# Kernel optimization log

Measured on AMD Instinct MI355X. Metric: run time of the kernel, lower is better.

The kernel has to match this reference:

```python
import jax, jax.numpy as jnp
import numpy as np

N = 400000   # active voxels (submanifold: N' == N)
K3 = 27      # kernel_size**3
D = 64       # in_channels
DP = 64      # out_channels


def setup_inputs() -> dict:
    key = jax.random.key(0)
    k1, k2, k3 = jax.random.split(key, 3)
    feats = jax.random.normal(k1, (N, D), dtype=jnp.float32)
    # neighbor index table: indices[k, n] = row of feats contributing at kernel
    # offset k for output site n; negative would mean 'no neighbor' (masked).
    indices = jax.random.randint(k2, (K3, N), 0, N, dtype=jnp.int64)
    weight = jax.random.normal(k3, (K3, D, DP), dtype=jnp.float32)
    return {"feats": feats, "indices": indices, "weight": weight}


def reference(feats, indices, weight):
    # Submanifold sparse conv as implicit GEMM:
    #   out[n] = sum_k feats[indices[k, n]] @ weight[k]   (skip indices < 0)
    # Scan over the K^3 kernel offsets (fixed, small) to avoid materializing
    # the full [K3, N, D] gathered tensor.
    n_out = indices.shape[1]
    dp = weight.shape[2]

    def body(acc, kw):
        idx, w = kw                                   # idx: [N'], w: [D, DP]
        valid = (idx >= 0)[:, None]                   # [N', 1]
        g = jnp.where(valid, feats[jnp.maximum(idx, 0)], 0.0)  # [N', D]
        return acc + g @ w, None

    init = jnp.zeros((n_out, dp), dtype=feats.dtype)
    out, _ = jax.lax.scan(body, init, (indices, weight))
    return out
```

## Files before the change

kernel.cpp:

```cpp
#include <hip/hip_runtime.h>
#include <hip/hip_bf16.h>
#include <stdint.h>

typedef __bf16 bf16_t;
typedef bf16_t bf16x8 __attribute__((ext_vector_type(8)));
typedef float f32x4 __attribute__((ext_vector_type(4)));

#define D_IN 64
#define D_OUT 64
#define BM 128
#define NTHREADS 512

#define GLOAD_LDS16(gsrc, ldst)                                                     \
    __builtin_amdgcn_global_load_lds(                                               \
        (const __attribute__((address_space(1))) uint32_t*)(gsrc),                  \
        (__attribute__((address_space(3))) uint32_t*)(ldst), 16, 0, 0)

__device__ __forceinline__ uint32_t swz(int row, int col) {
    return (uint32_t)((row * 128 + col * 2) ^ ((row & 7) << 4));
}

__global__ void convert_feats(const float* __restrict__ feats,
                              bf16_t* __restrict__ fb,
                              int n_elems , int total8 ) {
    int g = blockIdx.x * blockDim.x + threadIdx.x;
    for (; g < total8; g += gridDim.x * blockDim.x) {
        const int e = g * 8;
        bf16x8 v = {};
        if (e < n_elems) {
            f32x4 a = *(const f32x4*)(feats + e);
            f32x4 b = *(const f32x4*)(feats + e + 4);
            #pragma unroll
            for (int i = 0; i < 4; ++i) {
                v[i]     = (bf16_t)a[i];
                v[i + 4] = (bf16_t)b[i];
            }
        }
        *(bf16x8*)(fb + e) = v;
    }
}

__global__ void convert_weight(const float* __restrict__ w,
                               bf16_t* __restrict__ wtb, int k3) {
    const int k = blockIdx.x;
    const int tid = threadIdx.x;
    const int dp = tid >> 3;
    const int cp = tid & 7;
    const int d0 = (cp ^ (dp & 7)) * 8;
    const float* src = w + (size_t)k * (D_IN * D_OUT) + (size_t)d0 * D_OUT + dp;
    bf16x8 v;
    #pragma unroll
    for (int j = 0; j < 8; ++j) v[j] = (bf16_t)src[j * D_OUT];
    *(bf16x8*)((char*)wtb + (size_t)k * 8192 + tid * 16) = v;
}

__global__ __launch_bounds__(NTHREADS, 1) void subm_conv_mfma2(
    const bf16_t* __restrict__ fb,
    const int* __restrict__ indices,
    const bf16_t* __restrict__ wtb,
    float* __restrict__ out,
    int n_vox, int k3)
{
    __shared__ __align__(16) bf16_t As[2][BM * 64];
    __shared__ __align__(16) bf16_t Bs[2][64 * 64];

    const int tid  = threadIdx.x;
    const int lane = tid & 63;
    const int wv   = tid >> 6;
    const int l15  = lane & 15;
    const int l4   = lane >> 4;
    const int wr   = (wv >> 1) * 32;
    const int wc   = (wv & 1) * 32;
    const int n0   = blockIdx.x * BM;

    const int rA0 = wv * 16 + (lane >> 3);
    const int rA1 = rA0 + 8;
    const int cp  = lane & 7;
    const uint32_t so0 = (uint32_t)((cp ^ (rA0 & 7)) * 16);
    const uint32_t so1 = (uint32_t)((cp ^ (rA1 & 7)) * 16);

    int ia0 = -1, ia1 = -1;

    #define LOADIDX(kk) do {                                                   \
        const int* ip = indices + (size_t)(kk) * n_vox + n0;                   \
        ia0 = (n0 + rA0 < n_vox) ? ip[rA0] : -1;                               \
        ia1 = (n0 + rA1 < n_vox) ? ip[rA1] : -1;                               \
    } while (0)

    #define STAGE(buf, kk) do {                                                \
                      \
        GLOAD_LDS16((const char*)wtb + (size_t)(kk) * 8192 + tid * 16,         \
                    (char*)&Bs[buf][0] + wv * 1024);                           \
                                   \
        const size_t r0 = (size_t)((ia0 >= 0 && ia0 < n_vox) ? ia0 : n_vox);   \
        const size_t r1 = (size_t)((ia1 >= 0 && ia1 < n_vox) ? ia1 : n_vox);   \
        GLOAD_LDS16((const char*)fb + r0 * 128 + so0,                          \
                    (char*)&As[buf][0] + wv * 2048);                           \
        GLOAD_LDS16((const char*)fb + r1 * 128 + so1,                          \
                    (char*)&As[buf][0] + wv * 2048 + 1024);                    \
    } while (0)

    f32x4 acc[2][2];
    #pragma unroll
    for (int i = 0; i < 2; ++i)
        #pragma unroll
        for (int j = 0; j < 2; ++j)
            acc[i][j] = (f32x4){0.f, 0.f, 0.f, 0.f};

    LOADIDX(0);
    STAGE(0, 0);
    if (k3 > 1) LOADIDX(1);

    for (int k = 0; k < k3; ++k) {
        __syncthreads();

        if (k + 1 < k3) STAGE((k + 1) & 1, k + 1);
        if (k + 2 < k3) LOADIDX(k + 2);

        const char* ab = (const char*)&As[k & 1][0];
        const char* bb = (const char*)&Bs[k & 1][0];
        #pragma unroll
        for (int ks = 0; ks < 2; ++ks) {
            const int kc = ks * 32 + l4 * 8;
            bf16x8 a0 = *(const bf16x8*)(ab + swz(wr + l15,      kc));
            bf16x8 a1 = *(const bf16x8*)(ab + swz(wr + 16 + l15, kc));
            bf16x8 b0 = *(const bf16x8*)(bb + swz(wc + l15,      kc));
            bf16x8 b1 = *(const bf16x8*)(bb + swz(wc + 16 + l15, kc));
            acc[0][0] = __builtin_amdgcn_mfma_f32_16x16x32_bf16(a0, b0, acc[0][0], 0, 0, 0);
            acc[0][1] = __builtin_amdgcn_mfma_f32_16x16x32_bf16(a0, b1, acc[0][1], 0, 0, 0);
            acc[1][0] = __builtin_amdgcn_mfma_f32_16x16x32_bf16(a1, b0, acc[1][0], 0, 0, 0);
            acc[1][1] = __builtin_amdgcn_mfma_f32_16x16x32_bf16(a1, b1, acc[1][1], 0, 0, 0);
        }
    }

    #pragma unroll
    for (int mi = 0; mi < 2; ++mi)
        #pragma unroll
        for (int ni = 0; ni < 2; ++ni)
            #pragma unroll
            for (int j = 0; j < 4; ++j) {
                const int row = n0 + wr + mi * 16 + l4 * 4 + j;
                const int col = wc + ni * 16 + l15;
                if (row < n_vox)
                    out[(size_t)row * D_OUT + col] = acc[mi][ni][j];
            }
    #undef LOADIDX
    #undef STAGE
}

__global__ __launch_bounds__(NTHREADS, 1) void subm_conv_mfma_v1(
    const float* __restrict__ feats,
    const int* __restrict__ indices,
    const float* __restrict__ weight,
    float* __restrict__ out,
    int n_vox, int k3)
{
    __shared__ bf16_t As[BM * 64];
    __shared__ bf16_t Bs[64 * 64];

    const int tid  = threadIdx.x;
    const int lane = tid & 63;
    const int wv   = tid >> 6;
    const int wr   = (wv >> 1) * 32;
    const int wc   = (wv & 1) * 32;
    const int l15  = lane & 15;
    const int l4   = lane >> 4;
    const int n0   = blockIdx.x * BM;

    const int ar = tid >> 2;
    const int ac = (tid & 3) * 16;
    const int bdp = tid & 63;
    const int bd0 = (tid >> 6) * 8;

    f32x4 acc[2][2];
    #pragma unroll
    for (int i = 0; i < 2; ++i)
        #pragma unroll
        for (int j = 0; j < 2; ++j)
            acc[i][j] = (f32x4){0.f, 0.f, 0.f, 0.f};

    for (int k = 0; k < k3; ++k) {
        __syncthreads();
        {
            const int n = n0 + ar;
            int idx = (n < n_vox) ? indices[(size_t)k * n_vox + n] : -1;
            bf16x8 v0 = {}, v1 = {};
            if (idx >= 0) {
                const float* src = feats + (size_t)idx * D_IN + ac;
                f32x4 f0 = *(const f32x4*)(src + 0);
                f32x4 f1 = *(const f32x4*)(src + 4);
                f32x4 f2 = *(const f32x4*)(src + 8);
                f32x4 f3 = *(const f32x4*)(src + 12);
                #pragma unroll
                for (int i = 0; i < 4; ++i) {
                    v0[i]     = (bf16_t)f0[i];
                    v0[i + 4] = (bf16_t)f1[i];
                    v1[i]     = (bf16_t)f2[i];
                    v1[i + 4] = (bf16_t)f3[i];
                }
            }
            *(bf16x8*)((char*)As + swz(ar, ac))     = v0;
            *(bf16x8*)((char*)As + swz(ar, ac + 8)) = v1;
        }
        {
            const float* wsrc = weight + (size_t)k * (D_IN * D_OUT) + (size_t)bd0 * D_OUT + bdp;
            bf16x8 v;
            #pragma unroll
            for (int i = 0; i < 8; ++i) v[i] = (bf16_t)wsrc[i * D_OUT];
            *(bf16x8*)((char*)Bs + swz(bdp, bd0)) = v;
        }
        __syncthreads();
        #pragma unroll
        for (int ks = 0; ks < 2; ++ks) {
            const int kc = ks * 32 + l4 * 8;
            bf16x8 a0 = *(const bf16x8*)((char*)As + swz(wr + l15,      kc));
            bf16x8 a1 = *(const bf16x8*)((char*)As + swz(wr + 16 + l15, kc));
            bf16x8 b0 = *(const bf16x8*)((char*)Bs + swz(wc + l15,      kc));
            bf16x8 b1 = *(const bf16x8*)((char*)Bs + swz(wc + 16 + l15, kc));
            acc[0][0] = __builtin_amdgcn_mfma_f32_16x16x32_bf16(a0, b0, acc[0][0], 0, 0, 0);
            acc[0][1] = __builtin_amdgcn_mfma_f32_16x16x32_bf16(a0, b1, acc[0][1], 0, 0, 0);
            acc[1][0] = __builtin_amdgcn_mfma_f32_16x16x32_bf16(a1, b0, acc[1][0], 0, 0, 0);
            acc[1][1] = __builtin_amdgcn_mfma_f32_16x16x32_bf16(a1, b1, acc[1][1], 0, 0, 0);
        }
    }

    #pragma unroll
    for (int mi = 0; mi < 2; ++mi)
        #pragma unroll
        for (int ni = 0; ni < 2; ++ni)
            #pragma unroll
            for (int j = 0; j < 4; ++j) {
                const int row = n0 + wr + mi * 16 + l4 * 4 + j;
                const int col = wc + ni * 16 + l15;
                if (row < n_vox)
                    out[(size_t)row * D_OUT + col] = acc[mi][ni][j];
            }
}

extern "C" void kernel_launch(void* const* d_in, const int* in_sizes, int n_in,
                              void* d_out, int out_size, void* d_ws, size_t ws_size,
                              hipStream_t stream) {
    const float* feats   = (const float*)d_in[0];
    const int*   indices = (const int*)d_in[1];
    const float* weight  = (const float*)d_in[2];
    float* out = (float*)d_out;

    const int n_vox = in_sizes[0] / D_IN;
    const int k3    = in_sizes[2] / (D_IN * D_OUT);
    const int grid  = (n_vox + BM - 1) / BM;

    const size_t fb_bytes  = (size_t)(n_vox + 1) * D_IN * sizeof(bf16_t);
    const size_t fb_off    = 0;
    const size_t wtb_off   = (fb_bytes + 255) & ~(size_t)255;
    const size_t wtb_bytes = (size_t)k3 * 64 * 64 * sizeof(bf16_t);
    const size_t need      = wtb_off + wtb_bytes;

    if (ws_size >= need) {
        bf16_t* fb  = (bf16_t*)((char*)d_ws + fb_off);
        bf16_t* wtb = (bf16_t*)((char*)d_ws + wtb_off);

        const int n_elems = n_vox * D_IN;
        const int total8  = (n_vox + 1) * (D_IN / 8);
        int cblocks = (total8 + 255) / 256;
        if (cblocks > 2048) cblocks = 2048;
        convert_feats<<<cblocks, 256, 0, stream>>>(feats, fb, n_elems, total8);
        convert_weight<<<k3, 512, 0, stream>>>(weight, wtb, k3);
        subm_conv_mfma2<<<grid, NTHREADS, 0, stream>>>(fb, indices, wtb, out, n_vox, k3);
    } else {
        subm_conv_mfma_v1<<<grid, NTHREADS, 0, stream>>>(feats, indices, weight, out, n_vox, k3);
    }
}
```

Measured before the change: 245.0 us.

## Triple-buffer LDS staging with partial vmcnt waits and MFMA priority

Moves the gather-GEMM kernel from double to triple buffering of the A and B tiles in LDS. Index loads now run four offsets ahead and tile stages two ahead. The full __syncthreads is replaced by an explicit s_waitcnt vmcnt(5) plus a barrier, so later async loads can stay in flight, and s_setprio raises wave priority around the MFMA block. It also raises the launch-bounds occupancy hint to 4 blocks per CU. The aim is to hide more of the random-gather latency, at the cost of extra LDS (72KB per block), which may limit how many blocks fit, and reliance on a hand-counted vmcnt.

```diff
diff --git a/kernel.cpp b/kernel.cpp
--- a/kernel.cpp
+++ b/kernel.cpp
@@ -22,7 +22,7 @@
 
 __global__ void convert_feats(const float* __restrict__ feats,
                               bf16_t* __restrict__ fb,
-                              int n_elems , int total8 ) {
+                              int n_elems, int total8) {
     int g = blockIdx.x * blockDim.x + threadIdx.x;
     for (; g < total8; g += gridDim.x * blockDim.x) {
         const int e = g * 8;
@@ -54,15 +54,15 @@
     *(bf16x8*)((char*)wtb + (size_t)k * 8192 + tid * 16) = v;
 }
 
-__global__ __launch_bounds__(NTHREADS, 1) void subm_conv_mfma2(
+__global__ __launch_bounds__(NTHREADS, 4) void subm_conv_mfma3(
     const bf16_t* __restrict__ fb,
     const int* __restrict__ indices,
     const bf16_t* __restrict__ wtb,
     float* __restrict__ out,
     int n_vox, int k3)
 {
-    __shared__ __align__(16) bf16_t As[2][BM * 64];
-    __shared__ __align__(16) bf16_t Bs[2][64 * 64];
+    __shared__ __align__(16) bf16_t As[3][BM * 64];
+    __shared__ __align__(16) bf16_t Bs[3][64 * 64];
 
     const int tid  = threadIdx.x;
     const int lane = tid & 63;
@@ -79,25 +79,21 @@
     const uint32_t so0 = (uint32_t)((cp ^ (rA0 & 7)) * 16);
     const uint32_t so1 = (uint32_t)((cp ^ (rA1 & 7)) * 16);
 
-    int ia0 = -1, ia1 = -1;
-
-    #define LOADIDX(kk) do {                                                   \
+    #define LOADIDX(kk, j0, j1) do {                                           \
         const int* ip = indices + (size_t)(kk) * n_vox + n0;                   \
-        ia0 = (n0 + rA0 < n_vox) ? ip[rA0] : -1;                               \
-        ia1 = (n0 + rA1 < n_vox) ? ip[rA1] : -1;                               \
+        j0 = (n0 + rA0 < n_vox) ? ip[rA0] : -1;                                \
+        j1 = (n0 + rA1 < n_vox) ? ip[rA1] : -1;                                \
     } while (0)
 
-    #define STAGE(buf, kk) do {                                                \
-                      \
+    #define STAGE(bufi, kk, j0, j1) do {                                       \
         GLOAD_LDS16((const char*)wtb + (size_t)(kk) * 8192 + tid * 16,         \
-                    (char*)&Bs[buf][0] + wv * 1024);                           \
-                                   \
-        const size_t r0 = (size_t)((ia0 >= 0 && ia0 < n_vox) ? ia0 : n_vox);   \
-        const size_t r1 = (size_t)((ia1 >= 0 && ia1 < n_vox) ? ia1 : n_vox);   \
-        GLOAD_LDS16((const char*)fb + r0 * 128 + so0,                          \
-                    (char*)&As[buf][0] + wv * 2048);                           \
-        GLOAD_LDS16((const char*)fb + r1 * 128 + so1,                          \
-                    (char*)&As[buf][0] + wv * 2048 + 1024);                    \
+                    (char*)&Bs[(bufi)][0] + wv * 1024);                        \
+        const size_t r0_ = (size_t)(((j0) >= 0 && (j0) < n_vox) ? (j0) : n_vox); \
+        const size_t r1_ = (size_t)(((j1) >= 0 && (j1) < n_vox) ? (j1) : n_vox); \
+        GLOAD_LDS16((const char*)fb + r0_ * 128 + so0,                         \
+                    (char*)&As[(bufi)][0] + wv * 2048);                        \
+        GLOAD_LDS16((const char*)fb + r1_ * 128 + so1,                         \
+                    (char*)&As[(bufi)][0] + wv * 2048 + 1024);                 \
     } while (0)
 
     f32x4 acc[2][2];
@@ -107,18 +103,40 @@
         for (int j = 0; j < 2; ++j)
             acc[i][j] = (f32x4){0.f, 0.f, 0.f, 0.f};
 
-    LOADIDX(0);
-    STAGE(0, 0);
-    if (k3 > 1) LOADIDX(1);
+    {
+        int p00, p01, p10, p11;
+        LOADIDX(0, p00, p01);
+        const int k1 = (1 < k3) ? 1 : k3 - 1;
+        LOADIDX(k1, p10, p11);
+        STAGE(0, 0, p00, p01);
+        STAGE(1, k1, p10, p11);
+    }
+    int ia_c0, ia_c1, ia_n0, ia_n1;
+    {
+        const int k2 = (2 < k3) ? 2 : k3 - 1;
+        const int k3c = (3 < k3) ? 3 : k3 - 1;
+        LOADIDX(k2, ia_c0, ia_c1);
+        LOADIDX(k3c, ia_n0, ia_n1);
+    }
+
+    int bc = 0;
+    int bs = 2;
 
     for (int k = 0; k < k3; ++k) {
-        __syncthreads();
-
-        if (k + 1 < k3) STAGE((k + 1) & 1, k + 1);
-        if (k + 2 < k3) LOADIDX(k + 2);
-
-        const char* ab = (const char*)&As[k & 1][0];
-        const char* bb = (const char*)&Bs[k & 1][0];
+        asm volatile("s_waitcnt vmcnt(5)" ::: "memory");
+        __builtin_amdgcn_s_barrier();
+
+        int t0, t1;
+        {
+            const int ki = (k + 4 < k3) ? k + 4 : k3 - 1;
+            LOADIDX(ki, t0, t1);
+            const int ks = (k + 2 < k3) ? k + 2 : k3 - 1;
+            STAGE(bs, ks, ia_c0, ia_c1);
+        }
+
+        const char* ab = (const char*)&As[bc][0];
+        const char* bb = (const char*)&Bs[bc][0];
+        __builtin_amdgcn_s_setprio(1);
         #pragma unroll
         for (int ks = 0; ks < 2; ++ks) {
             const int kc = ks * 32 + l4 * 8;
@@ -131,6 +149,11 @@
             acc[1][0] = __builtin_amdgcn_mfma_f32_16x16x32_bf16(a1, b0, acc[1][0], 0, 0, 0);
             acc[1][1] = __builtin_amdgcn_mfma_f32_16x16x32_bf16(a1, b1, acc[1][1], 0, 0, 0);
         }
+        __builtin_amdgcn_s_setprio(0);
+
+        ia_c0 = ia_n0; ia_c1 = ia_n1; ia_n0 = t0; ia_n1 = t1;
+        bc = (bc == 2) ? 0 : bc + 1;
+        bs = (bs == 2) ? 0 : bs + 1;
     }
 
     #pragma unroll
@@ -250,13 +273,12 @@
     const int grid  = (n_vox + BM - 1) / BM;
 
     const size_t fb_bytes  = (size_t)(n_vox + 1) * D_IN * sizeof(bf16_t);
-    const size_t fb_off    = 0;
     const size_t wtb_off   = (fb_bytes + 255) & ~(size_t)255;
     const size_t wtb_bytes = (size_t)k3 * 64 * 64 * sizeof(bf16_t);
     const size_t need      = wtb_off + wtb_bytes;
 
-    if (ws_size >= need) {
-        bf16_t* fb  = (bf16_t*)((char*)d_ws + fb_off);
+    if (ws_size >= need && k3 >= 2) {
+        bf16_t* fb  = (bf16_t*)((char*)d_ws);
         bf16_t* wtb = (bf16_t*)((char*)d_ws + wtb_off);
 
         const int n_elems = n_vox * D_IN;
@@ -265,7 +287,7 @@
         if (cblocks > 2048) cblocks = 2048;
         convert_feats<<<cblocks, 256, 0, stream>>>(feats, fb, n_elems, total8);
         convert_weight<<<k3, 512, 0, stream>>>(weight, wtb, k3);
-        subm_conv_mfma2<<<grid, NTHREADS, 0, stream>>>(fb, indices, wtb, out, n_vox, k3);
+        subm_conv_mfma3<<<grid, NTHREADS, 0, stream>>>(fb, indices, wtb, out, n_vox, k3);
     } else {
         subm_conv_mfma_v1<<<grid, NTHREADS, 0, stream>>>(feats, indices, weight, out, n_vox, k3);
     }
```

Measured after the change: 284.3 us. 1.16x slower.

## Read weight fragments directly from global memory instead of staging through LDS

Applied to the files above, without the earlier changes.

Drops the LDS double buffer for the weight tile. Each wave now loads its B fragments straight from a row-major bf16 weight layout in global memory (likely L2-resident) at the start of each offset iteration. The convert kernel writes that unswizzled layout. This halves LDS traffic and footprint, so launch bounds go to 8 blocks per CU for more occupancy. The cost is redundant global or L2 reads of weights by every block and wave, plus tighter register limits from the higher occupancy bound.

```diff
diff --git a/kernel.cpp b/kernel.cpp
--- a/kernel.cpp
+++ b/kernel.cpp
@@ -22,7 +22,7 @@
 
 __global__ void convert_feats(const float* __restrict__ feats,
                               bf16_t* __restrict__ fb,
-                              int n_elems , int total8 ) {
+                              int n_elems, int total8) {
     int g = blockIdx.x * blockDim.x + threadIdx.x;
     for (; g < total8; g += gridDim.x * blockDim.x) {
         const int e = g * 8;
@@ -41,28 +41,26 @@
 }
 
 __global__ void convert_weight(const float* __restrict__ w,
-                               bf16_t* __restrict__ wtb, int k3) {
+                               bf16_t* __restrict__ wt, int k3) {
     const int k = blockIdx.x;
     const int tid = threadIdx.x;
     const int dp = tid >> 3;
-    const int cp = tid & 7;
-    const int d0 = (cp ^ (dp & 7)) * 8;
+    const int d0 = (tid & 7) * 8;
     const float* src = w + (size_t)k * (D_IN * D_OUT) + (size_t)d0 * D_OUT + dp;
     bf16x8 v;
     #pragma unroll
     for (int j = 0; j < 8; ++j) v[j] = (bf16_t)src[j * D_OUT];
-    *(bf16x8*)((char*)wtb + (size_t)k * 8192 + tid * 16) = v;
-}
-
-__global__ __launch_bounds__(NTHREADS, 1) void subm_conv_mfma2(
+    *(bf16x8*)((char*)wt + (size_t)k * 8192 + dp * 128 + d0 * 2) = v;
+}
+
+__global__ __launch_bounds__(NTHREADS, 8) void subm_conv_hi(
     const bf16_t* __restrict__ fb,
     const int* __restrict__ indices,
-    const bf16_t* __restrict__ wtb,
+    const bf16_t* __restrict__ wt,
     float* __restrict__ out,
     int n_vox, int k3)
 {
     __shared__ __align__(16) bf16_t As[2][BM * 64];
-    __shared__ __align__(16) bf16_t Bs[2][64 * 64];
 
     const int tid  = threadIdx.x;
     const int lane = tid & 63;
@@ -88,15 +86,11 @@
     } while (0)
 
     #define STAGE(buf, kk) do {                                                \
-                      \
-        GLOAD_LDS16((const char*)wtb + (size_t)(kk) * 8192 + tid * 16,         \
-                    (char*)&Bs[buf][0] + wv * 1024);                           \
-                                   \
-        const size_t r0 = (size_t)((ia0 >= 0 && ia0 < n_vox) ? ia0 : n_vox);   \
-        const size_t r1 = (size_t)((ia1 >= 0 && ia1 < n_vox) ? ia1 : n_vox);   \
-        GLOAD_LDS16((const char*)fb + r0 * 128 + so0,                          \
+        const size_t r0_ = (size_t)((ia0 >= 0 && ia0 < n_vox) ? ia0 : n_vox);  \
+        const size_t r1_ = (size_t)((ia1 >= 0 && ia1 < n_vox) ? ia1 : n_vox);  \
+        GLOAD_LDS16((const char*)fb + r0_ * 128 + so0,                         \
                     (char*)&As[buf][0] + wv * 2048);                           \
-        GLOAD_LDS16((const char*)fb + r1 * 128 + so1,                          \
+        GLOAD_LDS16((const char*)fb + r1_ * 128 + so1,                         \
                     (char*)&As[buf][0] + wv * 2048 + 1024);                    \
     } while (0)
 
@@ -114,22 +108,35 @@
     for (int k = 0; k < k3; ++k) {
         __syncthreads();
 
+        const char* wb = (const char*)wt + (size_t)k * 8192
+                       + (size_t)(wc + l15) * 128 + l4 * 16;
+        bf16x8 b00 = *(const bf16x8*)(wb);
+        bf16x8 b01 = *(const bf16x8*)(wb + 64);
+        bf16x8 b10 = *(const bf16x8*)(wb + 2048);
+        bf16x8 b11 = *(const bf16x8*)(wb + 2048 + 64);
+        __builtin_amdgcn_sched_barrier(0);
+
         if (k + 1 < k3) STAGE((k + 1) & 1, k + 1);
         if (k + 2 < k3) LOADIDX(k + 2);
 
         const char* ab = (const char*)&As[k & 1][0];
-        const char* bb = (const char*)&Bs[k & 1][0];
-        #pragma unroll
-        for (int ks = 0; ks < 2; ++ks) {
-            const int kc = ks * 32 + l4 * 8;
+        {
+            const int kc = l4 * 8;
             bf16x8 a0 = *(const bf16x8*)(ab + swz(wr + l15,      kc));
             bf16x8 a1 = *(const bf16x8*)(ab + swz(wr + 16 + l15, kc));
-            bf16x8 b0 = *(const bf16x8*)(bb + swz(wc + l15,      kc));
-            bf16x8 b1 = *(const bf16x8*)(bb + swz(wc + 16 + l15, kc));
-            acc[0][0] = __builtin_amdgcn_mfma_f32_16x16x32_bf16(a0, b0, acc[0][0], 0, 0, 0);
-            acc[0][1] = __builtin_amdgcn_mfma_f32_16x16x32_bf16(a0, b1, acc[0][1], 0, 0, 0);
-            acc[1][0] = __builtin_amdgcn_mfma_f32_16x16x32_bf16(a1, b0, acc[1][0], 0, 0, 0);
-            acc[1][1] = __builtin_amdgcn_mfma_f32_16x16x32_bf16(a1, b1, acc[1][1], 0, 0, 0);
+            acc[0][0] = __builtin_amdgcn_mfma_f32_16x16x32_bf16(a0, b00, acc[0][0], 0, 0, 0);
+            acc[0][1] = __builtin_amdgcn_mfma_f32_16x16x32_bf16(a0, b10, acc[0][1], 0, 0, 0);
+            acc[1][0] = __builtin_amdgcn_mfma_f32_16x16x32_bf16(a1, b00, acc[1][0], 0, 0, 0);
+            acc[1][1] = __builtin_amdgcn_mfma_f32_16x16x32_bf16(a1, b10, acc[1][1], 0, 0, 0);
+        }
+        {
+            const int kc = 32 + l4 * 8;
+            bf16x8 a0 = *(const bf16x8*)(ab + swz(wr + l15,      kc));
+            bf16x8 a1 = *(const bf16x8*)(ab + swz(wr + 16 + l15, kc));
+            acc[0][0] = __builtin_amdgcn_mfma_f32_16x16x32_bf16(a0, b01, acc[0][0], 0, 0, 0);
+            acc[0][1] = __builtin_amdgcn_mfma_f32_16x16x32_bf16(a0, b11, acc[0][1], 0, 0, 0);
+            acc[1][0] = __builtin_amdgcn_mfma_f32_16x16x32_bf16(a1, b01, acc[1][0], 0, 0, 0);
+            acc[1][1] = __builtin_amdgcn_mfma_f32_16x16x32_bf16(a1, b11, acc[1][1], 0, 0, 0);
         }
     }
 
@@ -148,14 +155,14 @@
     #undef STAGE
 }
 
-__global__ __launch_bounds__(NTHREADS, 1) void subm_conv_mfma_v1(
+__global__ __launch_bounds__(512, 1) void subm_conv_mfma_v1(
     const float* __restrict__ feats,
     const int* __restrict__ indices,
     const float* __restrict__ weight,
     float* __restrict__ out,
     int n_vox, int k3)
 {
-    __shared__ bf16_t As[BM * 64];
+    __shared__ bf16_t As[128 * 64];
     __shared__ bf16_t Bs[64 * 64];
 
     const int tid  = threadIdx.x;
@@ -165,7 +172,7 @@
     const int wc   = (wv & 1) * 32;
     const int l15  = lane & 15;
     const int l4   = lane >> 4;
-    const int n0   = blockIdx.x * BM;
+    const int n0   = blockIdx.x * 128;
 
     const int ar = tid >> 2;
     const int ac = (tid & 3) * 16;
@@ -250,23 +257,22 @@
     const int grid  = (n_vox + BM - 1) / BM;
 
     const size_t fb_bytes  = (size_t)(n_vox + 1) * D_IN * sizeof(bf16_t);
-    const size_t fb_off    = 0;
-    const size_t wtb_off   = (fb_bytes + 255) & ~(size_t)255;
-    const size_t wtb_bytes = (size_t)k3 * 64 * 64 * sizeof(bf16_t);
-    const size_t need      = wtb_off + wtb_bytes;
-
-    if (ws_size >= need) {
-        bf16_t* fb  = (bf16_t*)((char*)d_ws + fb_off);
-        bf16_t* wtb = (bf16_t*)((char*)d_ws + wtb_off);
+    const size_t wt_off    = (fb_bytes + 255) & ~(size_t)255;
+    const size_t wt_bytes  = (size_t)k3 * 64 * 64 * sizeof(bf16_t);
+    const size_t need      = wt_off + wt_bytes;
+
+    if (ws_size >= need && k3 >= 2) {
+        bf16_t* fb = (bf16_t*)((char*)d_ws);
+        bf16_t* wt = (bf16_t*)((char*)d_ws + wt_off);
 
         const int n_elems = n_vox * D_IN;
         const int total8  = (n_vox + 1) * (D_IN / 8);
         int cblocks = (total8 + 255) / 256;
         if (cblocks > 2048) cblocks = 2048;
         convert_feats<<<cblocks, 256, 0, stream>>>(feats, fb, n_elems, total8);
-        convert_weight<<<k3, 512, 0, stream>>>(weight, wtb, k3);
-        subm_conv_mfma2<<<grid, NTHREADS, 0, stream>>>(fb, indices, wtb, out, n_vox, k3);
+        convert_weight<<<k3, 512, 0, stream>>>(weight, wt, k3);
+        subm_conv_hi<<<grid, NTHREADS, 0, stream>>>(fb, indices, wt, out, n_vox, k3);
     } else {
-        subm_conv_mfma_v1<<<grid, NTHREADS, 0, stream>>>(feats, indices, weight, out, n_vox, k3);
-    }
-}
+        subm_conv_mfma_v1<<<grid, 512, 0, stream>>>(feats, indices, weight, out, n_vox, k3);
+    }
+}
```

Result: slower. 400.5 us (+63.5%).
